# Kernel optimization log

Hardware: AMD Instinct MI355X
Metric: run time of the kernel (lower is better)

The kernel has to match this reference:

```python
import jax, jax.numpy as jnp
import numpy as np

B, N = 262144, 64
CLIP_RATIO = 0.2
DUAL_CLIP = 5.0
USE_VALUE_CLIP = True
HALF_LOG_2PI = 0.5 * float(np.log(2.0 * np.pi))


def setup_inputs() -> dict:
    key = jax.random.key(0)
    ks = jax.random.split(key, 9)
    return {
        "mu_new": jax.random.normal(ks[0], (B, N), jnp.float32),
        "sigma_new": jax.random.uniform(ks[1], (B, N), jnp.float32, 0.5, 1.5),
        "mu_old": jax.random.normal(ks[2], (B, N), jnp.float32),
        "sigma_old": jax.random.uniform(ks[3], (B, N), jnp.float32, 0.5, 1.5),
        "action": jax.random.normal(ks[4], (B, N), jnp.float32),
        "value_new": jax.random.normal(ks[5], (B,), jnp.float32),
        "value_old": jax.random.normal(ks[6], (B,), jnp.float32),
        "adv": jax.random.normal(ks[7], (B,), jnp.float32),
        "return_": jax.random.normal(ks[8], (B,), jnp.float32),
        "weight": jnp.ones((B,), jnp.float32),
    }


def _gauss_logprob(action, mu, sigma):
    # independent Normal log-prob, summed over action dim -> (B,)
    z = (action - mu) / sigma
    return jnp.sum(-0.5 * z * z - jnp.log(sigma) - HALF_LOG_2PI, axis=-1)


def reference(mu_new, sigma_new, mu_old, sigma_old, action,
              value_new, value_old, adv, return_, weight):
    logp_new = _gauss_logprob(action, mu_new, sigma_new)   # (B,)
    logp_old = _gauss_logprob(action, mu_old, sigma_old)   # (B,) constant w.r.t. new params
    ratio = jnp.exp(logp_new - logp_old)

    surr1 = ratio * adv
    surr2 = jnp.clip(ratio, 1.0 - CLIP_RATIO, 1.0 + CLIP_RATIO) * adv
    clipped = jnp.minimum(surr1, surr2)
    # dual clip (arXiv:1912.09729 Eq. 5)
    clipped = jnp.maximum(clipped, DUAL_CLIP * adv)
    policy_loss = -jnp.mean(clipped * weight)

    # entropy of diagonal Gaussian, summed over N
    entropy = jnp.sum(0.5 + HALF_LOG_2PI + jnp.log(sigma_new), axis=-1)
    entropy_loss = jnp.mean(entropy * weight)

    if USE_VALUE_CLIP:
        value_clip = value_old + jnp.clip(value_new - value_old, -CLIP_RATIO, CLIP_RATIO)
        v1 = jnp.square(return_ - value_new)
        v2 = jnp.square(return_ - value_clip)
        value_loss = 0.5 * jnp.mean(jnp.maximum(v1, v2) * weight)
    else:
        value_loss = 0.5 * jnp.mean(jnp.square(return_ - value_new) * weight)

    approx_kl = jnp.mean(logp_old - logp_new)
    clipfrac = jnp.mean((jnp.abs(ratio - 1.0) > CLIP_RATIO).astype(jnp.float32))
    return policy_loss, value_loss, entropy_loss, approx_kl, clipfrac
```

## Files before the change

### kernel.cpp

```cpp
#include <hip/hip_runtime.h>

static constexpr int   N_DIM        = 64;
static constexpr float HALF_LOG_2PI = 0.9189385332046727f;
static constexpr float CLIP_RATIO   = 0.2f;
static constexpr float DUAL_CLIP    = 5.0f;
static constexpr int   GRID         = 2048;
static constexpr float ENT_CONST    = (float)N_DIM * (0.5f + HALF_LOG_2PI);
static constexpr float ENT_C16      = ENT_CONST / 16.0f;

__device__ __forceinline__ void ppo_set(const float4& mn, const float4& sn,
                                        const float4& mo, const float4& so,
                                        const float4& a,
                                        float& en_out, float& d_out)
{
    float qn = 0.f, qo = 0.f, en = 0.f, eo = 0.f;
#define PPO_COMP(c) {                                        \
        float rn = __builtin_amdgcn_rcpf(sn.c);              \
        float zn = (a.c - mn.c) * rn;  qn += zn * zn;        \
        float ro = __builtin_amdgcn_rcpf(so.c);              \
        float zo = (a.c - mo.c) * ro;  qo += zo * zo;        \
        en += __logf(sn.c);  eo += __logf(so.c); }
    PPO_COMP(x) PPO_COMP(y) PPO_COMP(z) PPO_COMP(w)
#undef PPO_COMP
    en_out = en;
    d_out  = 0.5f * (qo - qn) + (eo - en);
}

__global__ __launch_bounds__(256) void ppo_main(
    const float* __restrict__ mu_new,
    const float* __restrict__ sg_new,
    const float* __restrict__ mu_old,
    const float* __restrict__ sg_old,
    const float* __restrict__ act,
    const float* __restrict__ vnew,
    const float* __restrict__ vold,
    const float* __restrict__ adv,
    const float* __restrict__ ret,
    const float* __restrict__ wgt,
    float* __restrict__ ws,
    int b_rows)
{
    const int t    = threadIdx.x;
    const int wave = t >> 6;
    const int lane = t & 63;
    const int sub  = lane >> 4;

    float accP = 0.f, accV = 0.f, accE = 0.f, accK = 0.f, accC = 0.f;

    {
        const int r = blockIdx.x * 256 + t;
        if (r < b_rows) {
            const float vn = vnew[r], vo = vold[r], rt = ret[r], w = wgt[r];
            const float vc = vo + fminf(fmaxf(vn - vo, -CLIP_RATIO), CLIP_RATIO);
            const float d1 = rt - vn, d2 = rt - vc;
            accV += fmaxf(d1 * d1, d2 * d2) * w;
        }
    }

    const int n_g = b_rows >> 5;
    for (int g = blockIdx.x; g < n_g; g += gridDim.x) {
        const int row0 = g * 32 + wave * 8;
        const int r0   = row0 + sub;
        const int r1   = r0 + 4;
        const int off0 = row0 * N_DIM + lane * 4;
        const int off1 = off0 + 4 * N_DIM;

        const float4 mn0 = *(const float4*)(mu_new + off0);
        const float4 sn0 = *(const float4*)(sg_new + off0);
        const float4 mo0 = *(const float4*)(mu_old + off0);
        const float4 so0 = *(const float4*)(sg_old + off0);
        const float4 a0  = *(const float4*)(act    + off0);
        const float4 mn1 = *(const float4*)(mu_new + off1);
        const float4 sn1 = *(const float4*)(sg_new + off1);
        const float4 mo1 = *(const float4*)(mu_old + off1);
        const float4 so1 = *(const float4*)(sg_old + off1);
        const float4 a1  = *(const float4*)(act    + off1);
        const float w0 = wgt[r0], ad0 = adv[r0];
        const float w1 = wgt[r1], ad1 = adv[r1];

        float en0, d0, en1, d1;
        ppo_set(mn0, sn0, mo0, so0, a0, en0, d0);
        ppo_set(mn1, sn1, mo1, so1, a1, en1, d1);

        accK -= (d0 + d1);
        accE += w0 * (en0 + ENT_C16) + w1 * (en1 + ENT_C16);

#pragma unroll
        for (int m = 1; m < 16; m <<= 1) {
            d0 += __shfl_xor(d0, m, 16);
            d1 += __shfl_xor(d1, m, 16);
        }

        {
            const float ratio = __expf(d0);
            const float rc = fminf(fmaxf(ratio, 1.f - CLIP_RATIO), 1.f + CLIP_RATIO);
            float cl = fminf(ratio * ad0, rc * ad0);
            cl = fmaxf(cl, DUAL_CLIP * ad0);
            accP += cl * w0;
            accC += (fabsf(ratio - 1.f) > CLIP_RATIO) ? 1.f : 0.f;
        }
        {
            const float ratio = __expf(d1);
            const float rc = fminf(fmaxf(ratio, 1.f - CLIP_RATIO), 1.f + CLIP_RATIO);
            float cl = fminf(ratio * ad1, rc * ad1);
            cl = fmaxf(cl, DUAL_CLIP * ad1);
            accP += cl * w1;
            accC += (fabsf(ratio - 1.f) > CLIP_RATIO) ? 1.f : 0.f;
        }
    }

    accP *= 0.0625f;
    accC *= 0.0625f;

#pragma unroll
    for (int m = 1; m < 64; m <<= 1) {
        accP += __shfl_xor(accP, m, 64);
        accV += __shfl_xor(accV, m, 64);
        accE += __shfl_xor(accE, m, 64);
        accK += __shfl_xor(accK, m, 64);
        accC += __shfl_xor(accC, m, 64);
    }

    __shared__ float red[4][5];
    if (lane == 0) {
        red[wave][0] = accP; red[wave][1] = accV; red[wave][2] = accE;
        red[wave][3] = accK; red[wave][4] = accC;
    }
    __syncthreads();

    if (t == 0) {
        float s[5] = {0.f, 0.f, 0.f, 0.f, 0.f};
#pragma unroll
        for (int wv = 0; wv < 4; ++wv)
#pragma unroll
            for (int k = 0; k < 5; ++k) s[k] += red[wv][k];
#pragma unroll
        for (int k = 0; k < 5; ++k) ws[k * GRID + blockIdx.x] = s[k];
    }
}

__global__ __launch_bounds__(320) void ppo_reduce(
    const float* __restrict__ ws, float* __restrict__ out, int b_rows)
{
    const int wave = threadIdx.x >> 6;
    const int lane = threadIdx.x & 63;

    float v = 0.f;
    for (int i = lane; i < GRID; i += 64) v += ws[wave * GRID + i];
#pragma unroll
    for (int m = 1; m < 64; m <<= 1) v += __shfl_xor(v, m, 64);

    if (lane == 0) {
        const float invB = 1.0f / (float)b_rows;
        float o;
        if      (wave == 0) o = -v * invB;
        else if (wave == 1) o = 0.5f * v * invB;
        else                o = v * invB;
        out[wave] = o;
    }
}

extern "C" void kernel_launch(void* const* d_in, const int* in_sizes, int n_in,
                              void* d_out, int out_size, void* d_ws, size_t ws_size,
                              hipStream_t stream) {
    const float* mu_new = (const float*)d_in[0];
    const float* sg_new = (const float*)d_in[1];
    const float* mu_old = (const float*)d_in[2];
    const float* sg_old = (const float*)d_in[3];
    const float* act    = (const float*)d_in[4];
    const float* vnew   = (const float*)d_in[5];
    const float* vold   = (const float*)d_in[6];
    const float* adv    = (const float*)d_in[7];
    const float* ret    = (const float*)d_in[8];
    const float* wgt    = (const float*)d_in[9];
    float* out = (float*)d_out;
    float* ws  = (float*)d_ws;

    const int b_rows = in_sizes[5];

    ppo_main<<<GRID, 256, 0, stream>>>(mu_new, sg_new, mu_old, sg_old, act,
                                       vnew, vold, adv, ret, wgt,
                                       ws, b_rows);
    ppo_reduce<<<1, 320, 0, stream>>>(ws, out, b_rows);
}
```

Before: 317.0 us.

## Software-pipeline row-set loads and merge per-component logs into one log

The main loop now walks 4-row sets per wave with a two-stage register double buffer, issuing the next set's loads before computing the current one, so memory latency can overlap arithmetic. Log-sigma sums are computed as one log of the product of four sigmas instead of four logs, which cuts transcendental work. It also adds an occupancy hint to launch bounds. The double buffer raises register use, and the product-then-log form trades a little precision and overflow headroom for fewer instructions.

```diff
diff --git a/kernel.cpp b/kernel.cpp
--- a/kernel.cpp
+++ b/kernel.cpp
@@ -13,20 +13,39 @@
                                         const float4& a,
                                         float& en_out, float& d_out)
 {
-    float qn = 0.f, qo = 0.f, en = 0.f, eo = 0.f;
+    float qn = 0.f, qo = 0.f;
+    float pn = 1.f, po = 1.f;
 #define PPO_COMP(c) {                                        \
         float rn = __builtin_amdgcn_rcpf(sn.c);              \
         float zn = (a.c - mn.c) * rn;  qn += zn * zn;        \
         float ro = __builtin_amdgcn_rcpf(so.c);              \
         float zo = (a.c - mo.c) * ro;  qo += zo * zo;        \
-        en += __logf(sn.c);  eo += __logf(so.c); }
+        pn *= sn.c;  po *= so.c; }
     PPO_COMP(x) PPO_COMP(y) PPO_COMP(z) PPO_COMP(w)
 #undef PPO_COMP
+    const float en = __logf(pn);
+    const float eo = __logf(po);
     en_out = en;
     d_out  = 0.5f * (qo - qn) + (eo - en);
 }
 
-__global__ __launch_bounds__(256) void ppo_main(
+__device__ __forceinline__ void ppo_tail(float en, float d, float w, float ad,
+                                         float& accP, float& accE,
+                                         float& accK, float& accC)
+{
+    accK -= d;
+    accE += w * (en + ENT_C16);
+#pragma unroll
+    for (int m = 1; m < 16; m <<= 1) d += __shfl_xor(d, m, 16);
+    const float ratio = __expf(d);
+    const float rc = fminf(fmaxf(ratio, 1.f - CLIP_RATIO), 1.f + CLIP_RATIO);
+    float cl = fminf(ratio * ad, rc * ad);
+    cl = fmaxf(cl, DUAL_CLIP * ad);
+    accP += cl * w;
+    accC += (fabsf(ratio - 1.f) > CLIP_RATIO) ? 1.f : 0.f;
+}
+
+__global__ __launch_bounds__(256, 4) void ppo_main(
     const float* __restrict__ mu_new,
     const float* __restrict__ sg_new,
     const float* __restrict__ mu_old,
@@ -57,57 +76,44 @@
         }
     }
 
-    const int n_g = b_rows >> 5;
-    for (int g = blockIdx.x; g < n_g; g += gridDim.x) {
-        const int row0 = g * 32 + wave * 8;
-        const int r0   = row0 + sub;
-        const int r1   = r0 + 4;
-        const int off0 = row0 * N_DIM + lane * 4;
-        const int off1 = off0 + 4 * N_DIM;
+    const int n_sets = b_rows >> 2;
+    const int stride = gridDim.x << 2;
+    const int lofs   = lane * 4;
+    int s = (blockIdx.x << 2) + wave;
 
-        const float4 mn0 = *(const float4*)(mu_new + off0);
-        const float4 sn0 = *(const float4*)(sg_new + off0);
-        const float4 mo0 = *(const float4*)(mu_old + off0);
-        const float4 so0 = *(const float4*)(sg_old + off0);
-        const float4 a0  = *(const float4*)(act    + off0);
-        const float4 mn1 = *(const float4*)(mu_new + off1);
-        const float4 sn1 = *(const float4*)(sg_new + off1);
-        const float4 mo1 = *(const float4*)(mu_old + off1);
-        const float4 so1 = *(const float4*)(sg_old + off1);
-        const float4 a1  = *(const float4*)(act    + off1);
-        const float w0 = wgt[r0], ad0 = adv[r0];
-        const float w1 = wgt[r1], ad1 = adv[r1];
+#define PPO_LOAD(P) {                                            \
+        const int off = (s << 8) + lofs;                         \
+        const int r   = (s << 2) + sub;                          \
+        P##mn = *(const float4*)(mu_new + off);                  \
+        P##sn = *(const float4*)(sg_new + off);                  \
+        P##mo = *(const float4*)(mu_old + off);                  \
+        P##so = *(const float4*)(sg_old + off);                  \
+        P##a  = *(const float4*)(act    + off);                  \
+        P##w  = wgt[r];  P##ad = adv[r];                         \
+        s += stride; }
 
-        float en0, d0, en1, d1;
-        ppo_set(mn0, sn0, mo0, so0, a0, en0, d0);
-        ppo_set(mn1, sn1, mo1, so1, a1, en1, d1);
+#define PPO_COMPUTE(P) {                                         \
+        float en, d;                                             \
+        ppo_set(P##mn, P##sn, P##mo, P##so, P##a, en, d);        \
+        ppo_tail(en, d, P##w, P##ad, accP, accE, accK, accC); }
 
-        accK -= (d0 + d1);
-        accE += w0 * (en0 + ENT_C16) + w1 * (en1 + ENT_C16);
+    if (s < n_sets) {
+        float4 Amn, Asn, Amo, Aso, Aa;  float Aw, Aad;
+        float4 Bmn, Bsn, Bmo, Bso, Ba;  float Bw, Bad;
 
-#pragma unroll
-        for (int m = 1; m < 16; m <<= 1) {
-            d0 += __shfl_xor(d0, m, 16);
-            d1 += __shfl_xor(d1, m, 16);
+        PPO_LOAD(A);
+        bool pendA = true;
+        while (s < n_sets) {
+            PPO_LOAD(B);
+            PPO_COMPUTE(A);
+            pendA = false;
+            if (s < n_sets) { PPO_LOAD(A); pendA = true; }
+            PPO_COMPUTE(B);
         }
-
-        {
-            const float ratio = __expf(d0);
-            const float rc = fminf(fmaxf(ratio, 1.f - CLIP_RATIO), 1.f + CLIP_RATIO);
-            float cl = fminf(ratio * ad0, rc * ad0);
-            cl = fmaxf(cl, DUAL_CLIP * ad0);
-            accP += cl * w0;
-            accC += (fabsf(ratio - 1.f) > CLIP_RATIO) ? 1.f : 0.f;
-        }
-        {
-            const float ratio = __expf(d1);
-            const float rc = fminf(fmaxf(ratio, 1.f - CLIP_RATIO), 1.f + CLIP_RATIO);
-            float cl = fminf(ratio * ad1, rc * ad1);
-            cl = fmaxf(cl, DUAL_CLIP * ad1);
-            accP += cl * w1;
-            accC += (fabsf(ratio - 1.f) > CLIP_RATIO) ? 1.f : 0.f;
-        }
+        if (pendA) PPO_COMPUTE(A);
     }
+#undef PPO_LOAD
+#undef PPO_COMPUTE
 
     accP *= 0.0625f;
     accC *= 0.0625f;
@@ -129,13 +135,13 @@
     __syncthreads();
 
     if (t == 0) {
-        float s[5] = {0.f, 0.f, 0.f, 0.f, 0.f};
+        float sm[5] = {0.f, 0.f, 0.f, 0.f, 0.f};
 #pragma unroll
         for (int wv = 0; wv < 4; ++wv)
 #pragma unroll
-            for (int k = 0; k < 5; ++k) s[k] += red[wv][k];
+            for (int k = 0; k < 5; ++k) sm[k] += red[wv][k];
 #pragma unroll
-        for (int k = 0; k < 5; ++k) ws[k * GRID + blockIdx.x] = s[k];
+        for (int k = 0; k < 5; ++k) ws[k * GRID + blockIdx.x] = sm[k];
     }
 }
 
```

Result: no change. 316.0 us (-0.3%).
